# Kernel optimization log

Measured on AMD Instinct MI355X. Metric: run time of the kernel, lower is better.

The kernel has to match this reference:

```python
import jax, jax.numpy as jnp
import numpy as np

B, SQ, SK, DIM, HEADS, DH = 2, 1024, 1024, 512, 1, 64
INNER = HEADS * DH  # 64


def setup_inputs() -> dict:
    key = jax.random.key(0)
    ks = jax.random.split(key, 7)
    s = 0.05
    return {
        "x": jax.random.normal(ks[0], (B, SQ, DIM), jnp.float32),
        "emb": jax.random.normal(ks[1], (B, SK, DIM), jnp.float32),
        "Wq": jax.random.normal(ks[2], (DIM, INNER), jnp.float32) * s,
        "Wk": jax.random.normal(ks[3], (DIM, INNER), jnp.float32) * s,
        "Wv": jax.random.normal(ks[4], (DIM, INNER), jnp.float32) * s,
        "Wo": jax.random.normal(ks[5], (INNER, DIM), jnp.float32) * s,
        "bo": jnp.zeros((DIM,), jnp.float32),
    }


def reference(x, emb, Wq, Wk, Wv, Wo, bo):
    # QKV projections (bias-free Dense layers)
    q = x @ Wq     # [B, SQ, INNER]
    k = emb @ Wk   # [B, SK, INNER]
    v = emb @ Wv   # [B, SK, INNER]
    # Faithful to the module's reshape: (B, -1, inner_dim, heads).
    # With heads=1 the attention sees num_heads=INNER and q_features=heads=1.
    q = q.reshape(q.shape[0], -1, q.shape[-1], HEADS)  # [B, SQ, INNER, 1]
    k = k.reshape(k.shape[0], -1, k.shape[-1], HEADS)  # [B, SK, INNER, 1]
    v = v.reshape(v.shape[0], -1, v.shape[-1], HEADS)  # [B, SK, INNER, 1]
    # Memory-efficient attention scales q by q_features**-0.5 (here =1)
    scale = jnp.asarray(q.shape[-1], q.dtype) ** -0.5
    s = jnp.einsum('bqhd,bkhd->bqhk', q * scale, k)    # [B, SQ, INNER, SK]
    p = jax.nn.softmax(s, axis=-1)
    o = jnp.einsum('bqhk,bkhd->bqhd', p, v)            # [B, SQ, INNER, 1]
    o = o.reshape(x.shape[0], x.shape[1], -1)          # [B, SQ, INNER]
    return o @ Wo + bo                                 # [B, SQ, DIM]
```

## Files before the change

### kernel.cpp

```cpp
#include <hip/hip_runtime.h>
#include <hip/hip_bf16.h>

#define LOG2E 1.44269504088896340736f

__device__ __forceinline__ float fast_exp2(float x) {
#if __has_builtin(__builtin_amdgcn_exp2f)
    return __builtin_amdgcn_exp2f(x);
#else
    return exp2f(x);
#endif
}

typedef float f32x2 __attribute__((ext_vector_type(2)));

__device__ __forceinline__ f32x2 pk_fma(f32x2 a, f32x2 b, f32x2 c) {
#if __has_builtin(__builtin_elementwise_fma)
    return __builtin_elementwise_fma(a, b, c);
#else
    f32x2 r; r.x = fmaf(a.x, b.x, c.x); r.y = fmaf(a.y, b.y, c.y); return r;
#endif
}

__global__ __launch_bounds__(256) void proj_kernel(
    const float* __restrict__ x, const float* __restrict__ emb,
    const float* __restrict__ Wq, const float* __restrict__ Wk,
    const float* __restrict__ Wv,
    float* __restrict__ qT, float* __restrict__ kT, float* __restrict__ vT)
{
    __shared__ __align__(16) float sx[4096];
    __shared__ __align__(16) float sred[4096];
    const int t   = threadIdx.x;
    const int bid = blockIdx.x;
    const bool isQ = (bid < 256);
    const int rb  = isQ ? bid : (bid - 256);

    const float* src = (isQ ? x : emb) + (size_t)rb * 8 * 512;
    #pragma unroll
    for (int i = 0; i < 16; ++i) sx[i * 256 + t] = src[i * 256 + t];
    __syncthreads();

    const int b  = rb >> 7;
    const int q0 = (rb << 3) & 1023;

    if (isQ) {
        const int cp = (t & 31) * 2;
        const int g  = t >> 5;
        const int d0 = g * 64;
        float acc0[8], acc1[8];
        #pragma unroll
        for (int r = 0; r < 8; ++r) { acc0[r] = 0.f; acc1[r] = 0.f; }
        for (int dd = 0; dd < 64; dd += 4) {
            const int d = d0 + dd;
            float2 w0 = *(const float2*)&Wq[(d + 0) * 64 + cp];
            float2 w1 = *(const float2*)&Wq[(d + 1) * 64 + cp];
            float2 w2 = *(const float2*)&Wq[(d + 2) * 64 + cp];
            float2 w3 = *(const float2*)&Wq[(d + 3) * 64 + cp];
            #pragma unroll
            for (int r = 0; r < 8; ++r) {
                float4 xv = *(const float4*)&sx[r * 512 + d];
                acc0[r] = fmaf(xv.x, w0.x, acc0[r]); acc1[r] = fmaf(xv.x, w0.y, acc1[r]);
                acc0[r] = fmaf(xv.y, w1.x, acc0[r]); acc1[r] = fmaf(xv.y, w1.y, acc1[r]);
                acc0[r] = fmaf(xv.z, w2.x, acc0[r]); acc1[r] = fmaf(xv.z, w2.y, acc1[r]);
                acc0[r] = fmaf(xv.w, w3.x, acc0[r]); acc1[r] = fmaf(xv.w, w3.y, acc1[r]);
            }
        }
        #pragma unroll
        for (int r = 0; r < 8; ++r)
            *(float2*)&sred[g * 512 + r * 64 + cp] = make_float2(acc0[r], acc1[r]);
        __syncthreads();
        #pragma unroll
        for (int p = 0; p < 2; ++p) {
            int idx = p * 256 + t;
            int r = idx >> 6, h = idx & 63;
            float s = 0.f;
            #pragma unroll
            for (int g2 = 0; g2 < 8; ++g2) s += sred[g2 * 512 + r * 64 + h];
            qT[(size_t)(b * 64 + h) * 1024 + q0 + r] = s;
        }
    } else {
        const int cp = (t & 63) * 2;
        const int g  = t >> 6;
        const int d0 = g * 128;
        const float* Wsel = (cp < 64) ? (Wk + cp) : (Wv + (cp - 64));
        float acc0[8], acc1[8];
        #pragma unroll
        for (int r = 0; r < 8; ++r) { acc0[r] = 0.f; acc1[r] = 0.f; }
        for (int dd = 0; dd < 128; dd += 4) {
            const int d = d0 + dd;
            float2 w0 = *(const float2*)&Wsel[(d + 0) * 64];
            float2 w1 = *(const float2*)&Wsel[(d + 1) * 64];
            float2 w2 = *(const float2*)&Wsel[(d + 2) * 64];
            float2 w3 = *(const float2*)&Wsel[(d + 3) * 64];
            #pragma unroll
            for (int r = 0; r < 8; ++r) {
                float4 xv = *(const float4*)&sx[r * 512 + d];
                acc0[r] = fmaf(xv.x, w0.x, acc0[r]); acc1[r] = fmaf(xv.x, w0.y, acc1[r]);
                acc0[r] = fmaf(xv.y, w1.x, acc0[r]); acc1[r] = fmaf(xv.y, w1.y, acc1[r]);
                acc0[r] = fmaf(xv.z, w2.x, acc0[r]); acc1[r] = fmaf(xv.z, w2.y, acc1[r]);
                acc0[r] = fmaf(xv.w, w3.x, acc0[r]); acc1[r] = fmaf(xv.w, w3.y, acc1[r]);
            }
        }
        #pragma unroll
        for (int r = 0; r < 8; ++r)
            *(float2*)&sred[g * 1024 + r * 128 + cp] = make_float2(acc0[r], acc1[r]);
        __syncthreads();
        #pragma unroll
        for (int p = 0; p < 4; ++p) {
            int idx = p * 256 + t;
            int r = idx >> 7, c = idx & 127;
            float s = 0.f;
            #pragma unroll
            for (int g2 = 0; g2 < 4; ++g2) s += sred[g2 * 1024 + r * 128 + c];
            if (c < 64) kT[(size_t)(b * 64 + c) * 1024 + q0 + r] = s;
            else        vT[(size_t)(b * 64 + (c - 64)) * 1024 + q0 + r] = s;
        }
    }
}

__global__ __launch_bounds__(256) void attn_kernel(
    const float* __restrict__ qT, const float* __restrict__ kT,
    const float* __restrict__ vT, float* __restrict__ numP,
    float* __restrict__ denP)
{
    __shared__ __align__(16) float kc[512];
    __shared__ __align__(16) float vc[512];
    __shared__ float wred[8];
    const int t   = threadIdx.x;
    const int bid = blockIdx.x;
    const int b   = bid >> 9;
    const int h   = (bid >> 3) & 63;
    const int qq  = (bid >> 1) & 3;
    const int jh  = bid & 1;
    const size_t base = (size_t)(b * 64 + h) * 1024;

    float kmx = -1e30f, kmn = 1e30f;
    #pragma unroll
    for (int i = 0; i < 4; ++i) {
        float kv = kT[base + i * 256 + t];
        kmx = fmaxf(kmx, kv);
        kmn = fminf(kmn, kv);
        if ((i >> 1) == jh) kc[(i & 1) * 256 + t] = kv;
    }
    #pragma unroll
    for (int i2 = 0; i2 < 2; ++i2)
        vc[i2 * 256 + t] = vT[base + (jh * 2 + i2) * 256 + t];
    #pragma unroll
    for (int off = 32; off >= 1; off >>= 1) {
        kmx = fmaxf(kmx, __shfl_xor(kmx, off));
        kmn = fminf(kmn, __shfl_xor(kmn, off));
    }
    const int wid = t >> 6;
    if ((t & 63) == 0) { wred[wid] = kmx; wred[4 + wid] = kmn; }
    __syncthreads();
    kmx = fmaxf(fmaxf(wred[0], wred[1]), fmaxf(wred[2], wred[3]));
    kmn = fminf(fminf(wred[4], wred[5]), fminf(wred[6], wred[7]));

    const int q = qq * 256 + t;
    const float qs = qT[base + q];
    const float m  = (qs >= 0.f) ? qs * kmx : qs * kmn;
    const float a  = qs * LOG2E;
    const float bb = -m * LOG2E;
    const f32x2 a2 = { a, a };
    const f32x2 b2 = { bb, bb };

    f32x2 d01 = { 0.f, 0.f }, d23 = { 0.f, 0.f };
    f32x2 n01 = { 0.f, 0.f }, n23 = { 0.f, 0.f };
    const float4* kc4 = (const float4*)kc;
    const float4* vc4 = (const float4*)vc;
    for (int j = 0; j < 128; ++j) {
        float4 k4 = kc4[j];
        float4 v4 = vc4[j];
        f32x2 k01 = { k4.x, k4.y }, k23 = { k4.z, k4.w };
        f32x2 v01 = { v4.x, v4.y }, v23 = { v4.z, v4.w };
        f32x2 arg01 = pk_fma(a2, k01, b2);
        f32x2 arg23 = pk_fma(a2, k23, b2);
        f32x2 e01, e23;
        e01.x = fast_exp2(arg01.x); e01.y = fast_exp2(arg01.y);
        e23.x = fast_exp2(arg23.x); e23.y = fast_exp2(arg23.y);
        d01 += e01;
        d23 += e23;
        n01 = pk_fma(e01, v01, n01);
        n23 = pk_fma(e23, v23, n23);
    }
    const float den = (d01.x + d01.y) + (d23.x + d23.y);
    const float num = (n01.x + n01.y) + (n23.x + n23.y);
    const size_t p = (size_t)jh * 131072 + (size_t)(b * 1024 + q) * 64 + h;
    numP[p] = num;
    denP[p] = den;
}

__global__ __launch_bounds__(256) void oproj_kernel(
    const float* __restrict__ numP, const float* __restrict__ denP,
    const float* __restrict__ Wo, const float* __restrict__ bo,
    float* __restrict__ out)
{
    __shared__ __align__(16) float so[512];
    const int t  = threadIdx.x;
    const int rb = blockIdx.x;
    const size_t r0 = (size_t)rb * 8;
    #pragma unroll
    for (int p = 0; p < 2; ++p) {
        const size_t gi = r0 * 64 + p * 256 + t;
        float n = numP[gi] + numP[gi + 131072];
        float d = denP[gi] + denP[gi + 131072];
        so[p * 256 + t] = n / d;
    }
    __syncthreads();

    const int d2 = t * 2;
    float2 bv = *(const float2*)&bo[d2];
    float acc0[8], acc1[8];
    #pragma unroll
    for (int r = 0; r < 8; ++r) { acc0[r] = bv.x; acc1[r] = bv.y; }
    for (int hh = 0; hh < 64; hh += 4) {
        float2 w0 = *(const float2*)&Wo[(hh + 0) * 512 + d2];
        float2 w1 = *(const float2*)&Wo[(hh + 1) * 512 + d2];
        float2 w2 = *(const float2*)&Wo[(hh + 2) * 512 + d2];
        float2 w3 = *(const float2*)&Wo[(hh + 3) * 512 + d2];
        #pragma unroll
        for (int r = 0; r < 8; ++r) {
            float4 s4 = *(const float4*)&so[r * 64 + hh];
            acc0[r] = fmaf(s4.x, w0.x, acc0[r]); acc1[r] = fmaf(s4.x, w0.y, acc1[r]);
            acc0[r] = fmaf(s4.y, w1.x, acc0[r]); acc1[r] = fmaf(s4.y, w1.y, acc1[r]);
            acc0[r] = fmaf(s4.z, w2.x, acc0[r]); acc1[r] = fmaf(s4.z, w2.y, acc1[r]);
            acc0[r] = fmaf(s4.w, w3.x, acc0[r]); acc1[r] = fmaf(s4.w, w3.y, acc1[r]);
        }
    }
    #pragma unroll
    for (int r = 0; r < 8; ++r)
        *(float2*)&out[(r0 + r) * 512 + d2] = make_float2(acc0[r], acc1[r]);
}

extern "C" void kernel_launch(void* const* d_in, const int* in_sizes, int n_in,
                              void* d_out, int out_size, void* d_ws, size_t ws_size,
                              hipStream_t stream)
{
    const float* x   = (const float*)d_in[0];
    const float* emb = (const float*)d_in[1];
    const float* Wq  = (const float*)d_in[2];
    const float* Wk  = (const float*)d_in[3];
    const float* Wv  = (const float*)d_in[4];
    const float* Wo  = (const float*)d_in[5];
    const float* bo  = (const float*)d_in[6];
    float* out = (float*)d_out;

    float* qT   = (float*)d_ws;
    float* kT   = qT + 131072;
    float* vT   = kT + 131072;
    float* numP = vT + 131072;
    float* denP = numP + 262144;

    proj_kernel<<<512, 256, 0, stream>>>(x, emb, Wq, Wk, Wv, qT, kT, vT);
    attn_kernel<<<1024, 256, 0, stream>>>(qT, kT, vT, numP, denP);
    oproj_kernel<<<256, 256, 0, stream>>>(numP, denP, Wo, bo, out);
}
```

Measured before the change: 109.4 us.

## Split attention keys 8-way with 4 queries per thread; use packed FMA in projections

The attention kernel now splits each head's keys into eight 128-key chunks and has each thread handle four queries. Each LDS load of K and V is therefore reused across four queries, and the per-query inner loop becomes shorter. The cost is eight partial numerator/denominator buffers, larger workspace traffic, and an 8-way sum in the output projection. Separately, the projection and output GEMM inner loops switch from scalar fmaf to packed two-wide FMA, aiming to halve the FMA instruction count.

Result: slower. 112.6 us (+2.9%).

```diff
diff --git a/kernel.cpp b/kernel.cpp
--- a/kernel.cpp
+++ b/kernel.cpp
@@ -46,27 +46,29 @@
         const int cp = (t & 31) * 2;
         const int g  = t >> 5;
         const int d0 = g * 64;
-        float acc0[8], acc1[8];
-        #pragma unroll
-        for (int r = 0; r < 8; ++r) { acc0[r] = 0.f; acc1[r] = 0.f; }
+        f32x2 acc[8];
+        #pragma unroll
+        for (int r = 0; r < 8; ++r) acc[r] = (f32x2){0.f, 0.f};
         for (int dd = 0; dd < 64; dd += 4) {
             const int d = d0 + dd;
             float2 w0 = *(const float2*)&Wq[(d + 0) * 64 + cp];
             float2 w1 = *(const float2*)&Wq[(d + 1) * 64 + cp];
             float2 w2 = *(const float2*)&Wq[(d + 2) * 64 + cp];
             float2 w3 = *(const float2*)&Wq[(d + 3) * 64 + cp];
+            f32x2 w0p = {w0.x, w0.y}, w1p = {w1.x, w1.y};
+            f32x2 w2p = {w2.x, w2.y}, w3p = {w3.x, w3.y};
             #pragma unroll
             for (int r = 0; r < 8; ++r) {
                 float4 xv = *(const float4*)&sx[r * 512 + d];
-                acc0[r] = fmaf(xv.x, w0.x, acc0[r]); acc1[r] = fmaf(xv.x, w0.y, acc1[r]);
-                acc0[r] = fmaf(xv.y, w1.x, acc0[r]); acc1[r] = fmaf(xv.y, w1.y, acc1[r]);
-                acc0[r] = fmaf(xv.z, w2.x, acc0[r]); acc1[r] = fmaf(xv.z, w2.y, acc1[r]);
-                acc0[r] = fmaf(xv.w, w3.x, acc0[r]); acc1[r] = fmaf(xv.w, w3.y, acc1[r]);
+                acc[r] = pk_fma((f32x2){xv.x, xv.x}, w0p, acc[r]);
+                acc[r] = pk_fma((f32x2){xv.y, xv.y}, w1p, acc[r]);
+                acc[r] = pk_fma((f32x2){xv.z, xv.z}, w2p, acc[r]);
+                acc[r] = pk_fma((f32x2){xv.w, xv.w}, w3p, acc[r]);
             }
         }
         #pragma unroll
         for (int r = 0; r < 8; ++r)
-            *(float2*)&sred[g * 512 + r * 64 + cp] = make_float2(acc0[r], acc1[r]);
+            *(float2*)&sred[g * 512 + r * 64 + cp] = make_float2(acc[r].x, acc[r].y);
         __syncthreads();
         #pragma unroll
         for (int p = 0; p < 2; ++p) {
@@ -82,27 +84,29 @@
         const int g  = t >> 6;
         const int d0 = g * 128;
         const float* Wsel = (cp < 64) ? (Wk + cp) : (Wv + (cp - 64));
-        float acc0[8], acc1[8];
-        #pragma unroll
-        for (int r = 0; r < 8; ++r) { acc0[r] = 0.f; acc1[r] = 0.f; }
+        f32x2 acc[8];
+        #pragma unroll
+        for (int r = 0; r < 8; ++r) acc[r] = (f32x2){0.f, 0.f};
         for (int dd = 0; dd < 128; dd += 4) {
             const int d = d0 + dd;
             float2 w0 = *(const float2*)&Wsel[(d + 0) * 64];
             float2 w1 = *(const float2*)&Wsel[(d + 1) * 64];
             float2 w2 = *(const float2*)&Wsel[(d + 2) * 64];
             float2 w3 = *(const float2*)&Wsel[(d + 3) * 64];
+            f32x2 w0p = {w0.x, w0.y}, w1p = {w1.x, w1.y};
+            f32x2 w2p = {w2.x, w2.y}, w3p = {w3.x, w3.y};
             #pragma unroll
             for (int r = 0; r < 8; ++r) {
                 float4 xv = *(const float4*)&sx[r * 512 + d];
-                acc0[r] = fmaf(xv.x, w0.x, acc0[r]); acc1[r] = fmaf(xv.x, w0.y, acc1[r]);
-                acc0[r] = fmaf(xv.y, w1.x, acc0[r]); acc1[r] = fmaf(xv.y, w1.y, acc1[r]);
-                acc0[r] = fmaf(xv.z, w2.x, acc0[r]); acc1[r] = fmaf(xv.z, w2.y, acc1[r]);
-                acc0[r] = fmaf(xv.w, w3.x, acc0[r]); acc1[r] = fmaf(xv.w, w3.y, acc1[r]);
+                acc[r] = pk_fma((f32x2){xv.x, xv.x}, w0p, acc[r]);
+                acc[r] = pk_fma((f32x2){xv.y, xv.y}, w1p, acc[r]);
+                acc[r] = pk_fma((f32x2){xv.z, xv.z}, w2p, acc[r]);
+                acc[r] = pk_fma((f32x2){xv.w, xv.w}, w3p, acc[r]);
             }
         }
         #pragma unroll
         for (int r = 0; r < 8; ++r)
-            *(float2*)&sred[g * 1024 + r * 128 + cp] = make_float2(acc0[r], acc1[r]);
+            *(float2*)&sred[g * 1024 + r * 128 + cp] = make_float2(acc[r].x, acc[r].y);
         __syncthreads();
         #pragma unroll
         for (int p = 0; p < 4; ++p) {
@@ -122,15 +126,14 @@
     const float* __restrict__ vT, float* __restrict__ numP,
     float* __restrict__ denP)
 {
-    __shared__ __align__(16) float kc[512];
-    __shared__ __align__(16) float vc[512];
+    __shared__ __align__(16) float kc[128];
+    __shared__ __align__(16) float vc[128];
     __shared__ float wred[8];
     const int t   = threadIdx.x;
     const int bid = blockIdx.x;
     const int b   = bid >> 9;
     const int h   = (bid >> 3) & 63;
-    const int qq  = (bid >> 1) & 3;
-    const int jh  = bid & 1;
+    const int je  = bid & 7;
     const size_t base = (size_t)(b * 64 + h) * 1024;
 
     float kmx = -1e30f, kmn = 1e30f;
@@ -139,11 +142,11 @@
         float kv = kT[base + i * 256 + t];
         kmx = fmaxf(kmx, kv);
         kmn = fminf(kmn, kv);
-        if ((i >> 1) == jh) kc[(i & 1) * 256 + t] = kv;
-    }
-    #pragma unroll
-    for (int i2 = 0; i2 < 2; ++i2)
-        vc[i2 * 256 + t] = vT[base + (jh * 2 + i2) * 256 + t];
+    }
+    if (t < 128) {
+        kc[t] = kT[base + je * 128 + t];
+        vc[t] = vT[base + je * 128 + t];
+    }
     #pragma unroll
     for (int off = 32; off >= 1; off >>= 1) {
         kmx = fmaxf(kmx, __shfl_xor(kmx, off));
@@ -155,38 +158,52 @@
     kmx = fmaxf(fmaxf(wred[0], wred[1]), fmaxf(wred[2], wred[3]));
     kmn = fminf(fminf(wred[4], wred[5]), fminf(wred[6], wred[7]));
 
-    const int q = qq * 256 + t;
-    const float qs = qT[base + q];
-    const float m  = (qs >= 0.f) ? qs * kmx : qs * kmn;
-    const float a  = qs * LOG2E;
-    const float bb = -m * LOG2E;
-    const f32x2 a2 = { a, a };
-    const f32x2 b2 = { bb, bb };
-
-    f32x2 d01 = { 0.f, 0.f }, d23 = { 0.f, 0.f };
-    f32x2 n01 = { 0.f, 0.f }, n23 = { 0.f, 0.f };
+    f32x2 a2[4], b2[4];
+    #pragma unroll
+    for (int iq = 0; iq < 4; ++iq) {
+        const float qs = qT[base + iq * 256 + t];
+        const float m  = (qs >= 0.f) ? qs * kmx : qs * kmn;
+        const float a  = qs * LOG2E;
+        const float bb = -m * LOG2E;
+        a2[iq] = (f32x2){a, a};
+        b2[iq] = (f32x2){bb, bb};
+    }
+
+    f32x2 d01[4], d23[4], n01[4], n23[4];
+    #pragma unroll
+    for (int iq = 0; iq < 4; ++iq) {
+        d01[iq] = (f32x2){0.f, 0.f}; d23[iq] = (f32x2){0.f, 0.f};
+        n01[iq] = (f32x2){0.f, 0.f}; n23[iq] = (f32x2){0.f, 0.f};
+    }
     const float4* kc4 = (const float4*)kc;
     const float4* vc4 = (const float4*)vc;
-    for (int j = 0; j < 128; ++j) {
+    for (int j = 0; j < 32; ++j) {
         float4 k4 = kc4[j];
         float4 v4 = vc4[j];
-        f32x2 k01 = { k4.x, k4.y }, k23 = { k4.z, k4.w };
-        f32x2 v01 = { v4.x, v4.y }, v23 = { v4.z, v4.w };
-        f32x2 arg01 = pk_fma(a2, k01, b2);
-        f32x2 arg23 = pk_fma(a2, k23, b2);
-        f32x2 e01, e23;
-        e01.x = fast_exp2(arg01.x); e01.y = fast_exp2(arg01.y);
-        e23.x = fast_exp2(arg23.x); e23.y = fast_exp2(arg23.y);
-        d01 += e01;
-        d23 += e23;
-        n01 = pk_fma(e01, v01, n01);
-        n23 = pk_fma(e23, v23, n23);
-    }
-    const float den = (d01.x + d01.y) + (d23.x + d23.y);
-    const float num = (n01.x + n01.y) + (n23.x + n23.y);
-    const size_t p = (size_t)jh * 131072 + (size_t)(b * 1024 + q) * 64 + h;
-    numP[p] = num;
-    denP[p] = den;
+        f32x2 k01 = {k4.x, k4.y}, k23 = {k4.z, k4.w};
+        f32x2 v01 = {v4.x, v4.y}, v23 = {v4.z, v4.w};
+        #pragma unroll
+        for (int iq = 0; iq < 4; ++iq) {
+            f32x2 arg01 = pk_fma(a2[iq], k01, b2[iq]);
+            f32x2 arg23 = pk_fma(a2[iq], k23, b2[iq]);
+            f32x2 e01, e23;
+            e01.x = fast_exp2(arg01.x); e01.y = fast_exp2(arg01.y);
+            e23.x = fast_exp2(arg23.x); e23.y = fast_exp2(arg23.y);
+            d01[iq] += e01;
+            d23[iq] += e23;
+            n01[iq] = pk_fma(e01, v01, n01[iq]);
+            n23[iq] = pk_fma(e23, v23, n23[iq]);
+        }
+    }
+    #pragma unroll
+    for (int iq = 0; iq < 4; ++iq) {
+        const float den = (d01[iq].x + d01[iq].y) + (d23[iq].x + d23[iq].y);
+        const float num = (n01[iq].x + n01[iq].y) + (n23[iq].x + n23[iq].y);
+        const int q = iq * 256 + t;
+        const size_t p = (size_t)je * 131072 + (size_t)(b * 1024 + q) * 64 + h;
+        numP[p] = num;
+        denP[p] = den;
+    }
 }
 
 __global__ __launch_bounds__(256) void oproj_kernel(
@@ -201,34 +218,40 @@
     #pragma unroll
     for (int p = 0; p < 2; ++p) {
         const size_t gi = r0 * 64 + p * 256 + t;
-        float n = numP[gi] + numP[gi + 131072];
-        float d = denP[gi] + denP[gi + 131072];
+        float n = 0.f, d = 0.f;
+        #pragma unroll
+        for (int jp = 0; jp < 8; ++jp) {
+            n += numP[gi + (size_t)jp * 131072];
+            d += denP[gi + (size_t)jp * 131072];
+        }
         so[p * 256 + t] = n / d;
     }
     __syncthreads();
 
     const int d2 = t * 2;
     float2 bv = *(const float2*)&bo[d2];
-    float acc0[8], acc1[8];
-    #pragma unroll
-    for (int r = 0; r < 8; ++r) { acc0[r] = bv.x; acc1[r] = bv.y; }
+    f32x2 acc[8];
+    #pragma unroll
+    for (int r = 0; r < 8; ++r) acc[r] = (f32x2){bv.x, bv.y};
     for (int hh = 0; hh < 64; hh += 4) {
         float2 w0 = *(const float2*)&Wo[(hh + 0) * 512 + d2];
         float2 w1 = *(const float2*)&Wo[(hh + 1) * 512 + d2];
         float2 w2 = *(const float2*)&Wo[(hh + 2) * 512 + d2];
         float2 w3 = *(const float2*)&Wo[(hh + 3) * 512 + d2];
+        f32x2 w0p = {w0.x, w0.y}, w1p = {w1.x, w1.y};
+        f32x2 w2p = {w2.x, w2.y}, w3p = {w3.x, w3.y};
         #pragma unroll
         for (int r = 0; r < 8; ++r) {
             float4 s4 = *(const float4*)&so[r * 64 + hh];
-            acc0[r] = fmaf(s4.x, w0.x, acc0[r]); acc1[r] = fmaf(s4.x, w0.y, acc1[r]);
-            acc0[r] = fmaf(s4.y, w1.x, acc0[r]); acc1[r] = fmaf(s4.y, w1.y, acc1[r]);
-            acc0[r] = fmaf(s4.z, w2.x, acc0[r]); acc1[r] = fmaf(s4.z, w2.y, acc1[r]);
-            acc0[r] = fmaf(s4.w, w3.x, acc0[r]); acc1[r] = fmaf(s4.w, w3.y, acc1[r]);
+            acc[r] = pk_fma((f32x2){s4.x, s4.x}, w0p, acc[r]);
+            acc[r] = pk_fma((f32x2){s4.y, s4.y}, w1p, acc[r]);
+            acc[r] = pk_fma((f32x2){s4.z, s4.z}, w2p, acc[r]);
+            acc[r] = pk_fma((f32x2){s4.w, s4.w}, w3p, acc[r]);
         }
     }
     #pragma unroll
     for (int r = 0; r < 8; ++r)
-        *(float2*)&out[(r0 + r) * 512 + d2] = make_float2(acc0[r], acc1[r]);
+        *(float2*)&out[(r0 + r) * 512 + d2] = make_float2(acc[r].x, acc[r].y);
 }
 
 extern "C" void kernel_launch(void* const* d_in, const int* in_sizes, int n_in,
@@ -248,7 +271,7 @@
     float* kT   = qT + 131072;
     float* vT   = kT + 131072;
     float* numP = vT + 131072;
-    float* denP = numP + 262144;
+    float* denP = numP + 8 * 131072;
 
     proj_kernel<<<512, 256, 0, stream>>>(x, emb, Wq, Wk, Wv, qT, kT, vT);
     attn_kernel<<<1024, 256, 0, stream>>>(qT, kT, vT, numP, denP);
```
